# Performance work log

Measured on AMD Instinct MI355X. Metric: run time of the kernel, lower is better.

Reference implementation:

```python
import jax, jax.numpy as jnp
import numpy as np

B, INPUT_DIM, HEAD = 16384, 1024, 8
DIM = INPUT_DIM // HEAD


def setup_inputs() -> dict:
    key = jax.random.key(0)
    k1, k2, kw1, kb1, kw2, kw3 = jax.random.split(key, 6)
    x1 = jax.random.normal(k1, (B, INPUT_DIM), dtype=jnp.float32)
    x2 = jax.random.normal(k2, (B, INPUT_DIM), dtype=jnp.float32)
    s = 1.0 / np.sqrt(DIM)
    W1 = jax.random.uniform(kw1, (HEAD, DIM), jnp.float32, -s, s)   # per-head Linear(dim,1) weight
    b1 = jax.random.uniform(kb1, (HEAD,), jnp.float32, -s, s)       # per-head Linear(dim,1) bias
    W2 = jax.random.uniform(kw2, (HEAD, DIM), jnp.float32, -s, s)   # per-head Linear(dim,1,bias=False)
    W3 = jax.random.uniform(kw3, (HEAD, DIM, DIM), jnp.float32, -s, s)  # per-head Linear(dim,dim) [out,in]
    return {"x1": x1, "x2": x2, "W1": W1, "b1": b1, "W2": W2, "W3": W3}


def reference(x1, x2, W1, b1, W2, W3):
    b = x1.shape[0]
    h1 = x1.reshape(b, HEAD, DIM)
    h2 = x2.reshape(b, HEAD, DIM)
    # per-head scalar linears: [b, head]
    t1 = jnp.einsum('bhd,hd->bh', h1, W1) + b1
    t2 = jnp.einsum('bhd,hd->bh', h2, W2)
    # diag(w3(x1_h) @ x2_h^T) == sum((x1_h @ W3_h^T) * x2_h, -1), batched over heads
    proj = jnp.einsum('bhi,hoi->bho', h1, W3)
    t3 = jnp.sum(proj * h2, axis=-1)
    return jnp.sum(t1 + t2 + t3, axis=1)  # [b]
```

## Files before the change

### kernel.cpp

```cpp
#include <hip/hip_runtime.h>


#define NB 16384
#define NHEAD 8
#define NDIM 128

typedef __attribute__((ext_vector_type(8))) short bf16x8;
typedef __attribute__((ext_vector_type(16))) float f32x16;

__global__ __launch_bounds__(512, 4) void bilinear_fused(
    const float* __restrict__ x1, const float* __restrict__ x2,
    const float* __restrict__ W1, const float* __restrict__ b1,
    const float* __restrict__ W2, const float* __restrict__ W3,
    float* __restrict__ out)
{
    const int tid = threadIdx.x;
    const int bid = blockIdx.x;
    const int w    = tid >> 6;
    const int l    = tid & 63;
    const int col  = l & 31;
    const int hi5  = l >> 5;
    const int h    = bid & 7;
    const int bw   = (bid >> 3) * 256 + w * 32;

    __shared__ short lhi[8][4][512];
    __shared__ short llo[8][4][512];

#pragma unroll
    for (int i = 0; i < 4; ++i) {
        const int s    = i * 512 + tid;
        const int lane = s & 63;
        const int nt   = (s >> 6) & 3;
        const int ks   = s >> 8;
        const int n    = nt * 32 + (lane & 31);
        const int k    = ks * 16 + (lane >> 5) * 8;
        const float* src = W3 + ((size_t)(h * NDIM + n)) * NDIM + k;
        const float4 a = *reinterpret_cast<const float4*>(src);
        const float4 b = *reinterpret_cast<const float4*>(src + 4);
        float xf[8] = {a.x, a.y, a.z, a.w, b.x, b.y, b.z, b.w};
        bf16x8 hi, lo;
#pragma unroll
        for (int j = 0; j < 8; ++j) {
            const unsigned u = __float_as_uint(xf[j]);
            hi[j] = (short)(u >> 16);
            const float hf = __uint_as_float(u & 0xffff0000u);
            lo[j] = (short)(__float_as_uint(xf[j] - hf) >> 16);
        }
        *reinterpret_cast<bf16x8*>(&lhi[ks][nt][lane * 8]) = hi;
        *reinterpret_cast<bf16x8*>(&llo[ks][nt][lane * 8]) = lo;
    }

    const float* __restrict__ w1base = W1 + h * NDIM;
    const float* __restrict__ x1row  = x1 + (size_t)(bw + col) * (NHEAD * NDIM)
                                          + h * NDIM + hi5 * 8;

    f32x16 acc[4];
#pragma unroll
    for (int nt = 0; nt < 4; ++nt) acc[nt] = (f32x16)0.f;
    float t1 = 0.f;

    __syncthreads();

#pragma unroll
    for (int ks = 0; ks < 8; ++ks) {
        const int kbase = ks * 16;

        bf16x8 ahi, alo;
        {
            const float4 a = *reinterpret_cast<const float4*>(x1row + kbase);
            const float4 b = *reinterpret_cast<const float4*>(x1row + kbase + 4);
            float xf[8] = {a.x, a.y, a.z, a.w, b.x, b.y, b.z, b.w};
#pragma unroll
            for (int j = 0; j < 8; ++j) {
                const float w1l = w1base[kbase + j];
                const float w1h = w1base[kbase + 8 + j];
                const unsigned u = __float_as_uint(xf[j]);
                ahi[j] = (short)(u >> 16);
                alo[j] = (short)(__float_as_uint(
                    xf[j] - __uint_as_float(u & 0xffff0000u)) >> 16);
                t1 += xf[j] * (hi5 ? w1h : w1l);
            }
        }

#pragma unroll
        for (int nt = 0; nt < 4; ++nt) {
            const bf16x8 bhi = *reinterpret_cast<const bf16x8*>(&lhi[ks][nt][l * 8]);
            const bf16x8 blo = *reinterpret_cast<const bf16x8*>(&llo[ks][nt][l * 8]);
            acc[nt] = __builtin_amdgcn_mfma_f32_32x32x16_bf16(ahi, bhi, acc[nt], 0, 0, 0);
            acc[nt] = __builtin_amdgcn_mfma_f32_32x32x16_bf16(alo, bhi, acc[nt], 0, 0, 0);
            acc[nt] = __builtin_amdgcn_mfma_f32_32x32x16_bf16(ahi, blo, acc[nt], 0, 0, 0);
        }
    }

    float w2v[4];
#pragma unroll
    for (int nt = 0; nt < 4; ++nt) w2v[nt] = W2[h * NDIM + nt * 32 + col];

    float cr[16];
#pragma unroll
    for (int reg = 0; reg < 16; ++reg) {
        const int row = (reg & 3) + 8 * (reg >> 2) + 4 * hi5;
        const float* x2p = x2 + (size_t)(bw + row) * (NHEAD * NDIM)
                              + h * NDIM + col;
        float s = 0.f;
#pragma unroll
        for (int nt = 0; nt < 4; ++nt)
            s += (acc[nt][reg] + w2v[nt]) * x2p[nt * 32];
        cr[reg] = s;
    }
#pragma unroll
    for (int m = 1; m < 32; m <<= 1)
#pragma unroll
        for (int reg = 0; reg < 16; ++reg)
            cr[reg] += __shfl_xor(cr[reg], m, 64);

    float tf = t1;
    tf += __shfl_xor(tf, 32, 64);
#pragma unroll
    for (int reg = 0; reg < 16; ++reg) {
        const int row = (reg & 3) + 8 * (reg >> 2) + 4 * hi5;
        cr[reg] += __shfl(tf, row, 64);
    }

    float outv = cr[0];
#pragma unroll
    for (int reg = 1; reg < 16; ++reg)
        if (col == reg) outv = cr[reg];
    if (col < 16) {
        const int row = (col & 3) + 8 * (col >> 2) + 4 * hi5;
        atomicAdd(&out[bw + row], outv + b1[h]);
    }
}

extern "C" void kernel_launch(void* const* d_in, const int* in_sizes, int n_in,
                              void* d_out, int out_size, void* d_ws, size_t ws_size,
                              hipStream_t stream) {
    const float* x1 = (const float*)d_in[0];
    const float* x2 = (const float*)d_in[1];
    const float* W1 = (const float*)d_in[2];
    const float* b1 = (const float*)d_in[3];
    const float* W2 = (const float*)d_in[4];
    const float* W3 = (const float*)d_in[5];
    float* out = (float*)d_out;

    hipMemsetAsync(out, 0, (size_t)NB * sizeof(float), stream);
    bilinear_fused<<<dim3(NB / 256 * NHEAD), dim3(512), 0, stream>>>(
        x1, x2, W1, b1, W2, W3, out);
}
```

Measured before the change: 43.83 us.

## Halve block size and stage W3 through shared memory in two K-halves

Blocks shrink from 512 to 256 threads, each covering 128 rows, so the grid doubles. The W3 head slice is now converted to hi/lo bf16 and staged in two 64-wide K halves, which halves shared memory per block. The W3 load pattern is also reordered so adjacent threads read contiguous rows. The aim is higher occupancy and some overlap of staging with MFMA work. The cost is that each head's W3 is loaded and split twice as often overall, with an extra barrier per block.

```diff
diff --git a/kernel.cpp b/kernel.cpp
--- a/kernel.cpp
+++ b/kernel.cpp
@@ -8,48 +8,24 @@
 typedef __attribute__((ext_vector_type(8))) short bf16x8;
 typedef __attribute__((ext_vector_type(16))) float f32x16;
 
-__global__ __launch_bounds__(512, 4) void bilinear_fused(
+__global__ __launch_bounds__(256, 4) void bilinear_fused(
     const float* __restrict__ x1, const float* __restrict__ x2,
     const float* __restrict__ W1, const float* __restrict__ b1,
     const float* __restrict__ W2, const float* __restrict__ W3,
     float* __restrict__ out)
 {
-    const int tid = threadIdx.x;
-    const int bid = blockIdx.x;
-    const int w    = tid >> 6;
+    const int tid  = threadIdx.x;
     const int l    = tid & 63;
     const int col  = l & 31;
     const int hi5  = l >> 5;
+    const int bid  = blockIdx.x;
     const int h    = bid & 7;
-    const int bw   = (bid >> 3) * 256 + w * 32;
+    const int bw   = (bid >> 3) * 128 + (tid >> 6) * 32;
 
-    __shared__ short lhi[8][4][512];
-    __shared__ short llo[8][4][512];
+    __shared__ short lhi[4][4][512];
+    __shared__ short llo[4][4][512];
 
-#pragma unroll
-    for (int i = 0; i < 4; ++i) {
-        const int s    = i * 512 + tid;
-        const int lane = s & 63;
-        const int nt   = (s >> 6) & 3;
-        const int ks   = s >> 8;
-        const int n    = nt * 32 + (lane & 31);
-        const int k    = ks * 16 + (lane >> 5) * 8;
-        const float* src = W3 + ((size_t)(h * NDIM + n)) * NDIM + k;
-        const float4 a = *reinterpret_cast<const float4*>(src);
-        const float4 b = *reinterpret_cast<const float4*>(src + 4);
-        float xf[8] = {a.x, a.y, a.z, a.w, b.x, b.y, b.z, b.w};
-        bf16x8 hi, lo;
-#pragma unroll
-        for (int j = 0; j < 8; ++j) {
-            const unsigned u = __float_as_uint(xf[j]);
-            hi[j] = (short)(u >> 16);
-            const float hf = __uint_as_float(u & 0xffff0000u);
-            lo[j] = (short)(__float_as_uint(xf[j] - hf) >> 16);
-        }
-        *reinterpret_cast<bf16x8*>(&lhi[ks][nt][lane * 8]) = hi;
-        *reinterpret_cast<bf16x8*>(&llo[ks][nt][lane * 8]) = lo;
-    }
-
+    const float* __restrict__ w3base = W3 + (size_t)h * NDIM * NDIM;
     const float* __restrict__ w1base = W1 + h * NDIM;
     const float* __restrict__ x1row  = x1 + (size_t)(bw + col) * (NHEAD * NDIM)
                                           + h * NDIM + hi5 * 8;
@@ -59,37 +35,63 @@
     for (int nt = 0; nt < 4; ++nt) acc[nt] = (f32x16)0.f;
     float t1 = 0.f;
 
-    __syncthreads();
+    for (int p = 0; p < 2; ++p) {
+#pragma unroll
+        for (int i = 0; i < 4; ++i) {
+            const int s   = i * 256 + tid;
+            const int n   = s >> 3;
+            const int k8l = s & 7;
+            const float* src = w3base + (size_t)n * NDIM + p * 64 + k8l * 8;
+            const float4 a = *reinterpret_cast<const float4*>(src);
+            const float4 b = *reinterpret_cast<const float4*>(src + 4);
+            float xf[8] = {a.x, a.y, a.z, a.w, b.x, b.y, b.z, b.w};
+            bf16x8 hi, lo;
+#pragma unroll
+            for (int j = 0; j < 8; ++j) {
+                const unsigned u = __float_as_uint(xf[j]);
+                hi[j] = (short)(u >> 16);
+                const float hf = __uint_as_float(u & 0xffff0000u);
+                lo[j] = (short)(__float_as_uint(xf[j] - hf) >> 16);
+            }
+            const int ksl  = k8l >> 1;
+            const int lane = (k8l & 1) * 32 + (n & 31);
+            const int nt   = n >> 5;
+            *reinterpret_cast<bf16x8*>(&lhi[ksl][nt][lane * 8]) = hi;
+            *reinterpret_cast<bf16x8*>(&llo[ksl][nt][lane * 8]) = lo;
+        }
+        __syncthreads();
 
 #pragma unroll
-    for (int ks = 0; ks < 8; ++ks) {
-        const int kbase = ks * 16;
+        for (int ksl = 0; ksl < 4; ++ksl) {
+            const int kbase = p * 64 + ksl * 16;
 
-        bf16x8 ahi, alo;
-        {
-            const float4 a = *reinterpret_cast<const float4*>(x1row + kbase);
-            const float4 b = *reinterpret_cast<const float4*>(x1row + kbase + 4);
-            float xf[8] = {a.x, a.y, a.z, a.w, b.x, b.y, b.z, b.w};
+            bf16x8 ahi, alo;
+            {
+                const float4 a = *reinterpret_cast<const float4*>(x1row + kbase);
+                const float4 b = *reinterpret_cast<const float4*>(x1row + kbase + 4);
+                float xf[8] = {a.x, a.y, a.z, a.w, b.x, b.y, b.z, b.w};
 #pragma unroll
-            for (int j = 0; j < 8; ++j) {
-                const float w1l = w1base[kbase + j];
-                const float w1h = w1base[kbase + 8 + j];
-                const unsigned u = __float_as_uint(xf[j]);
-                ahi[j] = (short)(u >> 16);
-                alo[j] = (short)(__float_as_uint(
-                    xf[j] - __uint_as_float(u & 0xffff0000u)) >> 16);
-                t1 += xf[j] * (hi5 ? w1h : w1l);
+                for (int j = 0; j < 8; ++j) {
+                    const float w1l = w1base[kbase + j];
+                    const float w1h = w1base[kbase + 8 + j];
+                    const unsigned u = __float_as_uint(xf[j]);
+                    ahi[j] = (short)(u >> 16);
+                    alo[j] = (short)(__float_as_uint(
+                        xf[j] - __uint_as_float(u & 0xffff0000u)) >> 16);
+                    t1 += xf[j] * (hi5 ? w1h : w1l);
+                }
+            }
+
+#pragma unroll
+            for (int nt = 0; nt < 4; ++nt) {
+                const bf16x8 bhi = *reinterpret_cast<const bf16x8*>(&lhi[ksl][nt][l * 8]);
+                const bf16x8 blo = *reinterpret_cast<const bf16x8*>(&llo[ksl][nt][l * 8]);
+                acc[nt] = __builtin_amdgcn_mfma_f32_32x32x16_bf16(ahi, bhi, acc[nt], 0, 0, 0);
+                acc[nt] = __builtin_amdgcn_mfma_f32_32x32x16_bf16(alo, bhi, acc[nt], 0, 0, 0);
+                acc[nt] = __builtin_amdgcn_mfma_f32_32x32x16_bf16(ahi, blo, acc[nt], 0, 0, 0);
             }
         }
-
-#pragma unroll
-        for (int nt = 0; nt < 4; ++nt) {
-            const bf16x8 bhi = *reinterpret_cast<const bf16x8*>(&lhi[ks][nt][l * 8]);
-            const bf16x8 blo = *reinterpret_cast<const bf16x8*>(&llo[ks][nt][l * 8]);
-            acc[nt] = __builtin_amdgcn_mfma_f32_32x32x16_bf16(ahi, bhi, acc[nt], 0, 0, 0);
-            acc[nt] = __builtin_amdgcn_mfma_f32_32x32x16_bf16(alo, bhi, acc[nt], 0, 0, 0);
-            acc[nt] = __builtin_amdgcn_mfma_f32_32x32x16_bf16(ahi, blo, acc[nt], 0, 0, 0);
-        }
+        if (p == 0) __syncthreads();
     }
 
     float w2v[4];
@@ -144,6 +146,6 @@
     float* out = (float*)d_out;
 
     hipMemsetAsync(out, 0, (size_t)NB * sizeof(float), stream);
-    bilinear_fused<<<dim3(NB / 256 * NHEAD), dim3(512), 0, stream>>>(
+    bilinear_fused<<<dim3(NB / 128 * NHEAD), dim3(256), 0, stream>>>(
         x1, x2, W1, b1, W2, W3, out);
 }
```

Result: faster. 37.98 us (-13.3%).
